# Optimization experiments

Measured on AMD Instinct MI355X. Metric: run time of the kernel, lower is better.

## Reference

```python
import jax
import jax.numpy as jnp
from jax import lax
import numpy as np

B, C, H, W = 32, 256, 64, 64
R = 16  # low-rank dim of random bias


def setup_inputs() -> dict:
    key = jax.random.key(0)
    ks = jax.random.split(key, 6)
    return {
        "x": jax.random.normal(ks[0], (B, C, H, W), dtype=jnp.float32),
        "x_mid": jax.random.normal(ks[1], (B, C, H, W), dtype=jnp.float32),
        "g_w": jax.random.normal(ks[2], (C, C, 3, 3), dtype=jnp.float32) * 0.02,
        "w_w": jax.random.normal(ks[3], (C, C, 1, 1), dtype=jnp.float32) * 0.02,
        "weight1": jax.random.normal(ks[4], (C, R), dtype=jnp.float32) * 0.1,
        "weight2": jax.random.normal(ks[5], (C, R), dtype=jnp.float32) * 0.1,
    }


def _conv(x, w, padding):
    return lax.conv_general_dilated(
        x, w, window_strides=(1, 1), padding=padding,
        dimension_numbers=("NCHW", "OIHW", "NCHW"))


def reference(x, x_mid, g_w, w_w, weight1, weight2):
    b, c, h, w = x.shape
    # value path: 3x3 conv on x_mid (padding 1 -> SAME)
    g_x = _conv(x_mid, g_w, "SAME")                       # [b,c,h,w]
    value = g_x.reshape(b, c, h * w)                       # [b,c,N]
    feats = x.reshape(b, c, h * w)                         # query == key == x
    # channel-channel similarity: [b,c,c]
    sim = jnp.einsum("bcn,bdn->bcd", feats, feats) * (c ** -0.5)
    random_map = weight1 @ weight2.T                        # [c,c] low-rank bias
    attn = jax.nn.softmax(sim + random_map[None, :, :], axis=-1)
    context = jnp.einsum("bcd,bdn->bcn", attn, value).reshape(b, c, h, w)
    return _conv(context, w_w, "VALID")                     # 1x1 conv
```

## Files before the change

kernel.cpp:

```cpp
#include <hip/hip_runtime.h>


#define NB 32
#define NC 256
#define NPIX 4096

typedef __attribute__((ext_vector_type(8))) short short8;
typedef __attribute__((ext_vector_type(16))) float floatx16;

typedef __attribute__((address_space(1))) const unsigned int guint;
typedef __attribute__((address_space(3))) unsigned int luint;

__device__ inline short f2bf(float f) {
    union { float f; unsigned u; } v; v.f = f;
    unsigned r = v.u + 0x7fffu + ((v.u >> 16) & 1u);
    return (short)(r >> 16);
}

__global__ __launch_bounds__(256) void rm_kernel(const float* __restrict__ w1,
                                                 const float* __restrict__ w2,
                                                 float* __restrict__ rm) {
    int idx = blockIdx.x * 256 + threadIdx.x;
    int c = idx >> 8, d = idx & 255;
    float s = 0.f;
#pragma unroll
    for (int r = 0; r < 16; r++) s += w1[c * 16 + r] * w2[d * 16 + r];
    rm[idx] = s;
}

__global__ __launch_bounds__(256) void cvt_bf16_kernel(const float* __restrict__ in,
                                                       short* __restrict__ out) {
    size_t i = ((size_t)blockIdx.x * 256 + threadIdx.x) * 8;
    float4 v0 = *(const float4*)&in[i];
    float4 v1 = *(const float4*)&in[i + 4];
    short8 s;
    s[0] = f2bf(v0.x); s[1] = f2bf(v0.y); s[2] = f2bf(v0.z); s[3] = f2bf(v0.w);
    s[4] = f2bf(v1.x); s[5] = f2bf(v1.y); s[6] = f2bf(v1.z); s[7] = f2bf(v1.w);
    *(short8*)&out[i] = s;
}

__global__ __launch_bounds__(256) void cvt_x_kernel(const float* __restrict__ x,
                                                    short* __restrict__ xt) {
    const int h = blockIdx.x;
    const int b = blockIdx.y;
    __shared__ short xls[64 * 256];
    const int tid = threadIdx.x;
    for (int i = tid; i < 4096; i += 256) {
        int ci = i >> 4, w4 = (i & 15) << 2;
        float4 v = *(const float4*)&x[(((size_t)(b * 256 + ci)) * 64 + h) * 64 + w4];
        xls[(w4 + 0) * 256 + ci] = f2bf(v.x);
        xls[(w4 + 1) * 256 + ci] = f2bf(v.y);
        xls[(w4 + 2) * 256 + ci] = f2bf(v.z);
        xls[(w4 + 3) * 256 + ci] = f2bf(v.w);
    }
    __syncthreads();
    uint4* dst = (uint4*)&xt[(((size_t)(b * 64 + h)) * 64) * 256];
    const uint4* src = (const uint4*)xls;
    for (int i = tid; i < 2048; i += 256) dst[i] = src[i];
}

__global__ __launch_bounds__(256) void cvt_w_kernel(const float* __restrict__ g_w,
                                                    short* __restrict__ wt) {
    int o = blockIdx.x * 256 + threadIdx.x;
    if (o >= 73728) return;
    int co_t = o / 18432;
    int rem  = o - co_t * 18432;
    int ci_b = rem / 1152;
    int rem2 = rem - ci_b * 1152;
    int tap  = rem2 / 128;
    int rem3 = rem2 - tap * 128;
    int ch   = rem3 >> 6, ls = rem3 & 63;
    int co = co_t * 64 + ch * 32 + (ls & 31);
    int ci0 = ci_b * 16 + (ls >> 5) * 8;
    short8 v;
#pragma unroll
    for (int j = 0; j < 8; j++)
        v[j] = f2bf(g_w[((size_t)co * 256 + ci0 + j) * 9 + tap]);
    *(short8*)&wt[(size_t)o * 8] = v;
}

__global__ __launch_bounds__(256) void conv_mfma(const short* __restrict__ xt,
                                                 const short* __restrict__ wt,
                                                 short* __restrict__ value_t) {
    const int h0  = blockIdx.x * 4;
    const int cot = blockIdx.y;
    const int b   = blockIdx.z;
    __shared__ short ws[2][9 * 2 * 64 * 8];
    __shared__ short xs[6 * 2 * 66 * 8];
    const int tid = threadIdx.x;
    const int wv = tid >> 6, lane = tid & 63;
    const int kh2 = lane >> 5, ln = lane & 31;

    int xr0, xw0, xh0_, xr1, xw1, xh1_, xr2, xw2, xh2_;
    {
        int i0 = tid;        xr0 = i0 >> 7; int r0 = i0 & 127; xw0 = r0 >> 1; xh0_ = r0 & 1;
        int i1 = tid + 256;  xr1 = i1 >> 7; int r1 = i1 & 127; xw1 = r1 >> 1; xh1_ = r1 & 1;
        int i2 = tid + 512;  xr2 = i2 >> 7; int r2 = i2 & 127; xw2 = r2 >> 1; xh2_ = r2 & 1;
    }
    const int xd0 = (xr0 * 2 + xh0_) * 66 + 1 + xw0;
    const int xd1 = (xr1 * 2 + xh1_) * 66 + 1 + xw1;
    const int xd2 = (xr2 * 2 + xh2_) * 66 + 1 + xw2;
    const int hin0 = h0 - 1 + xr0, hin1 = h0 - 1 + xr1, hin2 = h0 - 1 + xr2;

    const short* wsrc0 = wt + (size_t)(cot * 16) * 1152 * 8;

#define STAGE_W(c)                                                             \
    do {                                                                       \
        short* wsd = ws[(c) & 1];                                              \
        const short* wsg = wsrc0 + (size_t)(c) * 1152 * 8;                     \
        _Pragma("unroll")                                                      \
        for (int j = 0; j < 5; ++j) {                                          \
            int k = wv + 4 * j;                                                \
            if (k < 18)                                                        \
                __builtin_amdgcn_global_load_lds(                              \
                    (guint*)(wsg + (size_t)(k * 64 + lane) * 8),               \
                    (luint*)(wsd + k * 512), 16, 0, 0);                        \
        }                                                                      \
    } while (0)

    uint4 xv0, xv1, xv2;
#define LOAD_X(c)                                                              \
    do {                                                                       \
        xv0 = make_uint4(0, 0, 0, 0); xv1 = xv0; xv2 = xv0;                    \
        if ((unsigned)hin0 < 64u)                                              \
            xv0 = *(const uint4*)&xt[(((size_t)(b * 64 + hin0)) * 64 + xw0) * 256 + (c) * 16 + xh0_ * 8]; \
        if ((unsigned)hin1 < 64u)                                              \
            xv1 = *(const uint4*)&xt[(((size_t)(b * 64 + hin1)) * 64 + xw1) * 256 + (c) * 16 + xh1_ * 8]; \
        if ((unsigned)hin2 < 64u)                                              \
            xv2 = *(const uint4*)&xt[(((size_t)(b * 64 + hin2)) * 64 + xw2) * 256 + (c) * 16 + xh2_ * 8]; \
    } while (0)

    if (tid < 24) {
        int r = tid >> 2, half = (tid >> 1) & 1, side = tid & 1;
        ((uint4*)xs)[(r * 2 + half) * 66 + side * 65] = make_uint4(0, 0, 0, 0);
    }

    floatx16 acc00 = {}, acc01 = {}, acc10 = {}, acc11 = {};

    STAGE_W(0);
    LOAD_X(0);
    for (int cib = 0; cib < 16; ++cib) {
        __syncthreads();
        {
            uint4* xdst = (uint4*)xs;
            xdst[xd0] = xv0; xdst[xd1] = xv1; xdst[xd2] = xv2;
        }
        __syncthreads();
        if (cib < 15) {
            STAGE_W(cib + 1);
            LOAD_X(cib + 1);
        }

        const short* wsc = ws[cib & 1];
#pragma unroll
        for (int tap = 0; tap < 9; ++tap) {
            const int kh = tap / 3, kw = tap - kh * 3;
            const int r = wv + kh;
            short8 wf0 = *(const short8*)&wsc[((tap * 2 + 0) * 64 + lane) * 8];
            short8 wf1 = *(const short8*)&wsc[((tap * 2 + 1) * 64 + lane) * 8];
            short8 xf0 = *(const short8*)&xs[(((r * 2 + kh2) * 66) + kw + ln) * 8];
            short8 xf1 = *(const short8*)&xs[(((r * 2 + kh2) * 66) + kw + 32 + ln) * 8];
            acc00 = __builtin_amdgcn_mfma_f32_32x32x16_bf16(xf0, wf0, acc00, 0, 0, 0);
            acc01 = __builtin_amdgcn_mfma_f32_32x32x16_bf16(xf0, wf1, acc01, 0, 0, 0);
            acc10 = __builtin_amdgcn_mfma_f32_32x32x16_bf16(xf1, wf0, acc10, 0, 0, 0);
            acc11 = __builtin_amdgcn_mfma_f32_32x32x16_bf16(xf1, wf1, acc11, 0, 0, 0);
        }
    }
#undef LOAD_X
#undef STAGE_W

    const int h_out = h0 + wv;
    short* vt = value_t + ((size_t)(b * 4096 + h_out * 64)) * 256 + cot * 64;
#pragma unroll
    for (int reg = 0; reg < 16; ++reg) {
        int m = (reg & 3) + 8 * (reg >> 2) + 4 * kh2;
        vt[(size_t)m * 256 + ln]             = f2bf(acc00[reg]);
        vt[(size_t)m * 256 + 32 + ln]        = f2bf(acc01[reg]);
        vt[(size_t)(m + 32) * 256 + ln]      = f2bf(acc10[reg]);
        vt[(size_t)(m + 32) * 256 + 32 + ln] = f2bf(acc11[reg]);
    }
}

__global__ __launch_bounds__(128) void gemm_nt_bf16(const short* __restrict__ A,
                                                    const short* __restrict__ B,
                                                    float* __restrict__ C, int K,
                                                    long sA, long sB, long sC,
                                                    int ldc, int tilesN) {
    const int mt = blockIdx.x / tilesN, nt = blockIdx.x % tilesN;
    A += (size_t)blockIdx.y * sA;
    B += (size_t)blockIdx.y * sB;
    C += (size_t)blockIdx.y * sC;
    const int wv = threadIdx.x >> 6, l = threadIdx.x & 63;
    const int ln = l & 31, kh = l >> 5;
    const short* arow = A + (size_t)(mt * 64 + wv * 32 + ln) * K + kh * 8;
    const short* brow = B + (size_t)(nt * 128 + ln) * K + kh * 8;
    floatx16 acc0 = {}, acc1 = {}, acc2 = {}, acc3 = {};
#pragma unroll 2
    for (int k0 = 0; k0 < K; k0 += 16) {
        short8 a  = *(const short8*)&arow[k0];
        short8 b0 = *(const short8*)&brow[k0];
        short8 b1 = *(const short8*)&brow[(size_t)32 * K + k0];
        short8 b2 = *(const short8*)&brow[(size_t)64 * K + k0];
        short8 b3 = *(const short8*)&brow[(size_t)96 * K + k0];
        acc0 = __builtin_amdgcn_mfma_f32_32x32x16_bf16(a, b0, acc0, 0, 0, 0);
        acc1 = __builtin_amdgcn_mfma_f32_32x32x16_bf16(a, b1, acc1, 0, 0, 0);
        acc2 = __builtin_amdgcn_mfma_f32_32x32x16_bf16(a, b2, acc2, 0, 0, 0);
        acc3 = __builtin_amdgcn_mfma_f32_32x32x16_bf16(a, b3, acc3, 0, 0, 0);
    }
    const int n0 = nt * 128;
#pragma unroll
    for (int reg = 0; reg < 16; ++reg) {
        int m = mt * 64 + wv * 32 + (reg & 3) + 8 * (reg >> 2) + 4 * kh;
        float* crow = C + (size_t)m * ldc + n0 + ln;
        crow[0]  = acc0[reg];
        crow[32] = acc1[reg];
        crow[64] = acc2[reg];
        crow[96] = acc3[reg];
    }
}

template <int BT, int OB>
__global__ __launch_bounds__(256) void gemm64(const float* __restrict__ A,
                                              const float* __restrict__ B,
                                              float* __restrict__ C, int K,
                                              long sA, long sB, long sC,
                                              int ldA, int ldB, int ldC, int tilesN) {
    const int m0 = (blockIdx.x / tilesN) * 64;
    const int n0 = (blockIdx.x % tilesN) * 64;
    A += (size_t)blockIdx.y * sA;
    B += (size_t)blockIdx.y * sB;
    const size_t coff = (size_t)blockIdx.y * sC;
    __shared__ float As[16][68], Bs[16][68];
    const int tid = threadIdx.x;
    const int tx = tid & 15, ty = tid >> 4;
    const int mm = tid >> 2, kk4 = (tid & 3) * 4;
    float acc[4][4] = {};

    for (int k0 = 0; k0 < K; k0 += 16) {
        __syncthreads();
        {
            float4 a = *(const float4*)&A[(size_t)(m0 + mm) * ldA + k0 + kk4];
            As[kk4 + 0][mm] = a.x; As[kk4 + 1][mm] = a.y;
            As[kk4 + 2][mm] = a.z; As[kk4 + 3][mm] = a.w;
        }
        if (BT) {
            float4 bv = *(const float4*)&B[(size_t)(n0 + mm) * ldB + k0 + kk4];
            Bs[kk4 + 0][mm] = bv.x; Bs[kk4 + 1][mm] = bv.y;
            Bs[kk4 + 2][mm] = bv.z; Bs[kk4 + 3][mm] = bv.w;
        } else {
            int bk = tid >> 4, bn = (tid & 15) * 4;
            *(float4*)&Bs[bk][bn] = *(const float4*)&B[(size_t)(k0 + bk) * ldB + n0 + bn];
        }
        __syncthreads();
#pragma unroll
        for (int kk = 0; kk < 16; kk++) {
            float4 a = *(float4*)&As[kk][ty * 4];
            float4 bv = *(float4*)&Bs[kk][tx * 4];
            float av[4] = {a.x, a.y, a.z, a.w};
            float bb[4] = {bv.x, bv.y, bv.z, bv.w};
#pragma unroll
            for (int i = 0; i < 4; i++)
#pragma unroll
                for (int j = 0; j < 4; j++) acc[i][j] += av[i] * bb[j];
        }
    }
#pragma unroll
    for (int i = 0; i < 4; i++) {
        if (OB) {
            short* Cs = (short*)C + coff;
            short4 o;
            o.x = f2bf(acc[i][0]); o.y = f2bf(acc[i][1]);
            o.z = f2bf(acc[i][2]); o.w = f2bf(acc[i][3]);
            *(short4*)&Cs[(size_t)(m0 + ty * 4 + i) * ldC + n0 + tx * 4] = o;
        } else {
            float* Cf = (float*)C + coff;
            float4 o = make_float4(acc[i][0], acc[i][1], acc[i][2], acc[i][3]);
            *(float4*)&Cf[(size_t)(m0 + ty * 4 + i) * ldC + n0 + tx * 4] = o;
        }
    }
}

__global__ __launch_bounds__(256) void softmax_kernel(float* __restrict__ sim,
                                                      const float* __restrict__ rm) {
    int row  = blockIdx.x * 4 + (threadIdx.x >> 6);
    int lane = threadIdx.x & 63;
    int c = row & 255;
    float4 v = *(float4*)&sim[(size_t)row * 256 + lane * 4];
    const float4 bias = *(const float4*)&rm[c * 256 + lane * 4];
    v.x = v.x * 0.0625f + bias.x;
    v.y = v.y * 0.0625f + bias.y;
    v.z = v.z * 0.0625f + bias.z;
    v.w = v.w * 0.0625f + bias.w;
    float m = fmaxf(fmaxf(v.x, v.y), fmaxf(v.z, v.w));
#pragma unroll
    for (int off = 32; off > 0; off >>= 1) m = fmaxf(m, __shfl_xor(m, off, 64));
    float e0 = __expf(v.x - m), e1 = __expf(v.y - m);
    float e2 = __expf(v.z - m), e3 = __expf(v.w - m);
    float s = e0 + e1 + e2 + e3;
#pragma unroll
    for (int off = 32; off > 0; off >>= 1) s += __shfl_xor(s, off, 64);
    float inv = 1.f / s;
    float4 o = make_float4(e0 * inv, e1 * inv, e2 * inv, e3 * inv);
    *(float4*)&sim[(size_t)row * 256 + lane * 4] = o;
}

extern "C" void kernel_launch(void* const* d_in, const int* in_sizes, int n_in,
                              void* d_out, int out_size, void* d_ws, size_t ws_size,
                              hipStream_t stream) {
    const float* x     = (const float*)d_in[0];
    const float* x_mid = (const float*)d_in[1];
    const float* g_w   = (const float*)d_in[2];
    const float* w_w   = (const float*)d_in[3];
    const float* w1    = (const float*)d_in[4];
    const float* w2    = (const float*)d_in[5];
    float* out = (float*)d_out;

    char* ws = (char*)d_ws;
    short* value_t = (short*)ws;
    float* sim     = (float*)(ws + (size_t)NB * NPIX * NC * 2);
    short* attn2_b = (short*)(sim + (size_t)NB * NC * NC);
    float* rm      = (float*)(attn2_b + (size_t)NB * NC * NC);
    short* xt      = (short*)(rm + NC * NC);
    short* xb      = xt + (size_t)NB * NPIX * NC;
    short* wt      = xb + (size_t)NB * NC * NPIX;

    cvt_w_kernel<<<288, 256, 0, stream>>>(g_w, wt);
    cvt_x_kernel<<<dim3(64, 32), 256, 0, stream>>>(x_mid, xt);
    cvt_bf16_kernel<<<16384, 256, 0, stream>>>(x, xb);
    rm_kernel<<<256, 256, 0, stream>>>(w1, w2, rm);
    conv_mfma<<<dim3(16, 4, 32), 256, 0, stream>>>(xt, wt, value_t);
    gemm_nt_bf16<<<dim3(8, 32), 128, 0, stream>>>(
        xb, xb, sim, 4096,
        (long)NC * NPIX, (long)NC * NPIX, (long)NC * NC, NC, 2);
    softmax_kernel<<<2048, 256, 0, stream>>>(sim, rm);
    gemm64<0, 1><<<dim3(16, 32), 256, 0, stream>>>(
        w_w, sim, (float*)attn2_b, 256,
        0L, (long)NC * NC, (long)NC * NC,
        NC, NC, NC, 4);
    gemm_nt_bf16<<<dim3(128, 32), 128, 0, stream>>>(
        attn2_b, value_t, out, 256,
        (long)NC * NC, (long)NPIX * NC, (long)NC * NPIX, NPIX, 32);
}
```

Baseline: 684.4 us.

## Stage conv weights via registers into single LDS buffer; widen final GEMM blocks

The 3x3 conv kernel stops using double-buffered direct global-to-LDS weight loads. It now prefetches the next channel block's weights and inputs into registers and writes them to a single shared buffer, which halves weight LDS use and may raise occupancy, at the cost of more registers and less overlap between loads and compute. The final attention-times-value GEMM moves to a new 512-thread kernel in which each block covers all 256 output rows for a 128-column tile, so the value rows are read from global memory once per tile rather than once per 64-row tile.

Result: no change. 676.9 us (-1.1%).

```diff
diff --git a/kernel.cpp b/kernel.cpp
--- a/kernel.cpp
+++ b/kernel.cpp
@@ -7,9 +7,6 @@
 
 typedef __attribute__((ext_vector_type(8))) short short8;
 typedef __attribute__((ext_vector_type(16))) float floatx16;
-
-typedef __attribute__((address_space(1))) const unsigned int guint;
-typedef __attribute__((address_space(3))) unsigned int luint;
 
 __device__ inline short f2bf(float f) {
     union { float f; unsigned u; } v; v.f = f;
@@ -85,7 +82,7 @@
     const int h0  = blockIdx.x * 4;
     const int cot = blockIdx.y;
     const int b   = blockIdx.z;
-    __shared__ short ws[2][9 * 2 * 64 * 8];
+    __shared__ short ws[9 * 2 * 64 * 8];
     __shared__ short xs[6 * 2 * 66 * 8];
     const int tid = threadIdx.x;
     const int wv = tid >> 6, lane = tid & 63;
@@ -101,26 +98,17 @@
     const int xd1 = (xr1 * 2 + xh1_) * 66 + 1 + xw1;
     const int xd2 = (xr2 * 2 + xh2_) * 66 + 1 + xw2;
     const int hin0 = h0 - 1 + xr0, hin1 = h0 - 1 + xr1, hin2 = h0 - 1 + xr2;
-
-    const short* wsrc0 = wt + (size_t)(cot * 16) * 1152 * 8;
-
-#define STAGE_W(c)                                                             \
+    const uint4* wsrc_base = (const uint4*)&wt[(size_t)(cot * 16) * 1152 * 8];
+
+    uint4 wr0, wr1, wr2, wr3, wr4;
+    uint4 xv0, xv1, xv2;
+
+#define LOAD_CIB(c)                                                            \
     do {                                                                       \
-        short* wsd = ws[(c) & 1];                                              \
-        const short* wsg = wsrc0 + (size_t)(c) * 1152 * 8;                     \
-        _Pragma("unroll")                                                      \
-        for (int j = 0; j < 5; ++j) {                                          \
-            int k = wv + 4 * j;                                                \
-            if (k < 18)                                                        \
-                __builtin_amdgcn_global_load_lds(                              \
-                    (guint*)(wsg + (size_t)(k * 64 + lane) * 8),               \
-                    (luint*)(wsd + k * 512), 16, 0, 0);                        \
-        }                                                                      \
-    } while (0)
-
-    uint4 xv0, xv1, xv2;
-#define LOAD_X(c)                                                              \
-    do {                                                                       \
+        const uint4* wsrc = wsrc_base + (size_t)(c) * 1152;                    \
+        wr0 = wsrc[tid];        wr1 = wsrc[tid + 256];                         \
+        wr2 = wsrc[tid + 512];  wr3 = wsrc[tid + 768];                         \
+        if (tid < 128) wr4 = wsrc[tid + 1024];                                 \
         xv0 = make_uint4(0, 0, 0, 0); xv1 = xv0; xv2 = xv0;                    \
         if ((unsigned)hin0 < 64u)                                              \
             xv0 = *(const uint4*)&xt[(((size_t)(b * 64 + hin0)) * 64 + xw0) * 256 + (c) * 16 + xh0_ * 8]; \
@@ -130,6 +118,16 @@
             xv2 = *(const uint4*)&xt[(((size_t)(b * 64 + hin2)) * 64 + xw2) * 256 + (c) * 16 + xh2_ * 8]; \
     } while (0)
 
+#define WRITE_LDS()                                                            \
+    do {                                                                       \
+        uint4* wdst = (uint4*)ws;                                              \
+        wdst[tid] = wr0;        wdst[tid + 256] = wr1;                         \
+        wdst[tid + 512] = wr2;  wdst[tid + 768] = wr3;                         \
+        if (tid < 128) wdst[tid + 1024] = wr4;                                 \
+        uint4* xdst = (uint4*)xs;                                              \
+        xdst[xd0] = xv0; xdst[xd1] = xv1; xdst[xd2] = xv2;                     \
+    } while (0)
+
     if (tid < 24) {
         int r = tid >> 2, half = (tid >> 1) & 1, side = tid & 1;
         ((uint4*)xs)[(r * 2 + half) * 66 + side * 65] = make_uint4(0, 0, 0, 0);
@@ -137,27 +135,19 @@
 
     floatx16 acc00 = {}, acc01 = {}, acc10 = {}, acc11 = {};
 
-    STAGE_W(0);
-    LOAD_X(0);
+    LOAD_CIB(0);
     for (int cib = 0; cib < 16; ++cib) {
         __syncthreads();
-        {
-            uint4* xdst = (uint4*)xs;
-            xdst[xd0] = xv0; xdst[xd1] = xv1; xdst[xd2] = xv2;
-        }
+        WRITE_LDS();
+        if (cib < 15) LOAD_CIB(cib + 1);
         __syncthreads();
-        if (cib < 15) {
-            STAGE_W(cib + 1);
-            LOAD_X(cib + 1);
-        }
-
-        const short* wsc = ws[cib & 1];
+
 #pragma unroll
         for (int tap = 0; tap < 9; ++tap) {
             const int kh = tap / 3, kw = tap - kh * 3;
             const int r = wv + kh;
-            short8 wf0 = *(const short8*)&wsc[((tap * 2 + 0) * 64 + lane) * 8];
-            short8 wf1 = *(const short8*)&wsc[((tap * 2 + 1) * 64 + lane) * 8];
+            short8 wf0 = *(const short8*)&ws[((tap * 2 + 0) * 64 + lane) * 8];
+            short8 wf1 = *(const short8*)&ws[((tap * 2 + 1) * 64 + lane) * 8];
             short8 xf0 = *(const short8*)&xs[(((r * 2 + kh2) * 66) + kw + ln) * 8];
             short8 xf1 = *(const short8*)&xs[(((r * 2 + kh2) * 66) + kw + 32 + ln) * 8];
             acc00 = __builtin_amdgcn_mfma_f32_32x32x16_bf16(xf0, wf0, acc00, 0, 0, 0);
@@ -166,8 +156,8 @@
             acc11 = __builtin_amdgcn_mfma_f32_32x32x16_bf16(xf1, wf1, acc11, 0, 0, 0);
         }
     }
-#undef LOAD_X
-#undef STAGE_W
+#undef LOAD_CIB
+#undef WRITE_LDS
 
     const int h_out = h0 + wv;
     short* vt = value_t + ((size_t)(b * 4096 + h_out * 64)) * 256 + cot * 64;
@@ -219,6 +209,43 @@
     }
 }
 
+__global__ __launch_bounds__(512) void gemm_bwide(const short* __restrict__ A,
+                                                  const short* __restrict__ B,
+                                                  float* __restrict__ C,
+                                                  long sA, long sB, long sC) {
+    const int nt = blockIdx.x;
+    A += (size_t)blockIdx.y * sA;
+    B += (size_t)blockIdx.y * sB;
+    C += (size_t)blockIdx.y * sC;
+    const int wid = threadIdx.x >> 6, l = threadIdx.x & 63;
+    const int ln = l & 31, kh = l >> 5;
+    const short* arow = A + (size_t)(wid * 32 + ln) * 256 + kh * 8;
+    const short* brow = B + (size_t)(nt * 128 + ln) * 256 + kh * 8;
+    floatx16 acc0 = {}, acc1 = {}, acc2 = {}, acc3 = {};
+#pragma unroll 2
+    for (int k0 = 0; k0 < 256; k0 += 16) {
+        short8 a  = *(const short8*)&arow[k0];
+        short8 b0 = *(const short8*)&brow[k0];
+        short8 b1 = *(const short8*)&brow[32 * 256 + k0];
+        short8 b2 = *(const short8*)&brow[64 * 256 + k0];
+        short8 b3 = *(const short8*)&brow[96 * 256 + k0];
+        acc0 = __builtin_amdgcn_mfma_f32_32x32x16_bf16(a, b0, acc0, 0, 0, 0);
+        acc1 = __builtin_amdgcn_mfma_f32_32x32x16_bf16(a, b1, acc1, 0, 0, 0);
+        acc2 = __builtin_amdgcn_mfma_f32_32x32x16_bf16(a, b2, acc2, 0, 0, 0);
+        acc3 = __builtin_amdgcn_mfma_f32_32x32x16_bf16(a, b3, acc3, 0, 0, 0);
+    }
+    const int n0 = nt * 128;
+#pragma unroll
+    for (int reg = 0; reg < 16; ++reg) {
+        int m = wid * 32 + (reg & 3) + 8 * (reg >> 2) + 4 * kh;
+        float* crow = C + (size_t)m * 4096 + n0 + ln;
+        crow[0]  = acc0[reg];
+        crow[32] = acc1[reg];
+        crow[64] = acc2[reg];
+        crow[96] = acc3[reg];
+    }
+}
+
 template <int BT, int OB>
 __global__ __launch_bounds__(256) void gemm64(const float* __restrict__ A,
                                               const float* __restrict__ B,
@@ -337,7 +364,7 @@
         w_w, sim, (float*)attn2_b, 256,
         0L, (long)NC * NC, (long)NC * NC,
         NC, NC, NC, 4);
-    gemm_nt_bf16<<<dim3(128, 32), 128, 0, stream>>>(
-        attn2_b, value_t, out, 256,
-        (long)NC * NC, (long)NPIX * NC, (long)NC * NPIX, NPIX, 32);
-}
+    gemm_bwide<<<dim3(32, 32), 512, 0, stream>>>(
+        attn2_b, value_t, out,
+        (long)NC * NC, (long)NPIX * NC, (long)NC * NPIX);
+}
```
